# Performance work log

Hardware: AMD Instinct MI355X
Metric: run time of the kernel (lower is better)

## Reference

```python
import jax, jax.numpy as jnp
import numpy as np

N_NODES = 50000
EPS = 1e-5


def sage_conv_max(x, src, dst, W_l, b_l, W_r):
    # PyG SAGEConv(aggr='max'): out = lin_l(max_j x_j) + lin_r(x_i)
    msg = x[src]                                   # [E, d] gather
    agg = jnp.full((x.shape[0], x.shape[1]), -jnp.inf, dtype=x.dtype)
    agg = agg.at[dst].max(msg)                     # scatter-max over edges
    agg = jnp.where(jnp.isneginf(agg), 0.0, agg)   # isolated nodes -> 0 (PyG convention)
    return agg @ W_l.T + b_l + x @ W_r.T


def batch_norm(x, gamma, beta):
    mean = jnp.mean(x, axis=0)
    var = jnp.var(x, axis=0)
    return (x - mean) * jax.lax.rsqrt(var + EPS) * gamma + beta


def setup_inputs() -> dict:
    key = jax.random.key(0)
    ks = jax.random.split(key, 10)
    d_in, d_h, d_out = 128, 128, 32
    s = lambda fan: 1.0 / np.sqrt(fan)
    return {
        "x": jax.random.normal(ks[0], (N_NODES, d_in), dtype=jnp.float32),
        "edge_index": jax.random.randint(ks[1], (2, 800000), 0, N_NODES, dtype=jnp.int32),
        "W_l1": jax.random.uniform(ks[2], (d_h, d_in), jnp.float32, -s(d_in), s(d_in)),
        "b_l1": jnp.zeros((d_h,), jnp.float32),
        "W_r1": jax.random.uniform(ks[3], (d_h, d_in), jnp.float32, -s(d_in), s(d_in)),
        "gamma1": jnp.ones((d_h,), jnp.float32),
        "beta1": jnp.zeros((d_h,), jnp.float32),
        "W_l2": jax.random.uniform(ks[4], (d_out, d_h), jnp.float32, -s(d_h), s(d_h)),
        "b_l2": jnp.zeros((d_out,), jnp.float32),
        "W_r2": jax.random.uniform(ks[5], (d_out, d_h), jnp.float32, -s(d_h), s(d_h)),
    }


def reference(x, edge_index, W_l1, b_l1, W_r1, gamma1, beta1, W_l2, b_l2, W_r2):
    src, dst = edge_index[0], edge_index[1]
    h = sage_conv_max(x, src, dst, W_l1, b_l1, W_r1)
    h = batch_norm(h, gamma1, beta1)
    h = jax.nn.relu(h)
    # dropout is identity at inference
    return sage_conv_max(h, src, dst, W_l2, b_l2, W_r2)
```

## Files before the change

### kernel.cpp

```cpp
#include <hip/hip_runtime.h>
#include <math.h>
#include <float.h>

#define N_NODES 50000
#define N_EDGES 800000
#define DH 128
#define NB 196
#define EB 4096
#define NBUCK 98
#define BSH 9
#define CAP 80
#define SEGC 9216
#define CELLS_PER_BUCKET (NB * CAP)

typedef __attribute__((ext_vector_type(8))) short bf16x8;
typedef __attribute__((ext_vector_type(4))) float f32x4;

static __device__ __forceinline__ unsigned short f2bf(float f) {
  unsigned int u = __float_as_uint(f);
  u = (u + 0x7fff + ((u >> 16) & 1)) >> 16;
  return (unsigned short)u;
}

__global__ __launch_bounds__(256) void setup_kernel(
    const int* __restrict__ src, const int* __restrict__ dst,
    unsigned int* __restrict__ pairs,
    const float* __restrict__ x, const float* __restrict__ Wl1,
    const float* __restrict__ Wr1, const float* __restrict__ Wl2,
    const float* __restrict__ Wr2, unsigned int* __restrict__ x_bf,
    unsigned short* __restrict__ Wcat1, unsigned short* __restrict__ Wcat2,
    float* __restrict__ gsums) {
  const int b = blockIdx.x, tid = threadIdx.x;
  if (b < NB) {
    __shared__ int cur[NBUCK];
    if (tid < NBUCK) cur[tid] = 0;
    __syncthreads();
#pragma unroll
    for (int it = 0; it < EB / 256; ++it) {
      int e = b * EB + it * 256 + tid;
      if (e < N_EDGES) {
        int d = dst[e];
        int bk = d >> BSH;
        int p = atomicAdd(&cur[bk], 1);
        if (p < CAP)
          pairs[(size_t)(bk * NB + b) * CAP + p] =
              (unsigned)src[e] | ((unsigned)(d & 511) << 16);
      }
    }
    __syncthreads();
    for (int s = tid; s < NBUCK * CAP; s += 256) {
      int bk = s / CAP, slot = s - bk * CAP;
      if (slot >= cur[bk])
        pairs[(size_t)(bk * NB + b) * CAP + slot] = 0x80000000u;
    }
  } else if (b < NB + 6250) {
    int i = (b - NB) * 256 + tid;
    float4 v = ((const float4*)x)[i];
    uint2 o;
    o.x = (unsigned int)f2bf(v.x) | ((unsigned int)f2bf(v.y) << 16);
    o.y = (unsigned int)f2bf(v.z) | ((unsigned int)f2bf(v.w) << 16);
    ((uint2*)x_bf)[i] = o;
  } else if (b < NB + 6410) {
    int i = (b - NB - 6250) * 256 + tid;
    if (i < 32768) {
      int n = i >> 8, k = i & 255;
      float w = (k < 128) ? Wl1[n * 128 + k] : Wr1[n * 128 + (k - 128)];
      Wcat1[i] = f2bf(w);
    } else if (i < 40960) {
      int j = i - 32768;
      int n = j >> 8, k = j & 255;
      float w = (k < 128) ? Wl2[n * 128 + k] : Wr2[n * 128 + (k - 128)];
      Wcat2[j] = f2bf(w);
    }
  } else {
#pragma unroll
    for (int i = 0; i < 8; ++i) gsums[i * 256 + tid] = 0.f;
  }
}

__global__ __launch_bounds__(1024) void bucket_sort(const unsigned int* __restrict__ pairs,
                                                    unsigned int* __restrict__ rowinfo,
                                                    int* __restrict__ elist) {
  __shared__ int hist[512], sc[512], cpos[512];
  const int b = blockIdx.x, tid = threadIdx.x;
  const size_t s0 = (size_t)b * CELLS_PER_BUCKET;
  if (tid < 512) hist[tid] = 0;
  __syncthreads();
  for (int p = tid; p < CELLS_PER_BUCKET; p += 1024) {
    unsigned int pr = pairs[s0 + p];
    if ((int)pr >= 0) atomicAdd(&hist[(pr >> 16) & 511], 1);
  }
  __syncthreads();
  if (tid < 512) sc[tid] = hist[tid];
  __syncthreads();
  for (int off = 1; off < 512; off <<= 1) {
    int x = (tid < 512 && tid >= off) ? sc[tid - off] : 0;
    __syncthreads();
    if (tid < 512) sc[tid] += x;
    __syncthreads();
  }
  if (tid < 512) {
    int excl = sc[tid] - hist[tid];
    cpos[tid] = excl;
    int node = (b << BSH) + tid;
    if (node < N_NODES)
      rowinfo[node] = (unsigned)(b * SEGC + excl) | ((unsigned)hist[tid] << 20);
  }
  __syncthreads();
  for (int p = tid; p < CELLS_PER_BUCKET; p += 1024) {
    unsigned int pr = pairs[s0 + p];
    if ((int)pr >= 0) {
      int loc = atomicAdd(&cpos[(pr >> 16) & 511], 1);
      elist[b * SEGC + loc] = (int)(pr & 0xffffu);
    }
  }
}

template <bool BN>
__global__ __launch_bounds__(256) void agg_max_bf16(const uint4* __restrict__ feat4,
                                                    const unsigned int* __restrict__ rowinfo,
                                                    const int* __restrict__ elist,
                                                    const float* __restrict__ gsums,
                                                    const float* __restrict__ gamma,
                                                    const float* __restrict__ beta,
                                                    uint4* __restrict__ out4) {
  __shared__ float s_scale[128], s_shift[128];
  if (BN) {
    int t = threadIdx.x;
    if (t < 128) {
      float sm = 0.f, sq = 0.f;
#pragma unroll
      for (int r = 0; r < 8; ++r) {
        sm += gsums[r * 256 + t];
        sq += gsums[r * 256 + 128 + t];
      }
      const float inv = 1.f / (float)N_NODES;
      float mean = sm * inv;
      float var = sq * inv - mean * mean;
      float sc = gamma[t] * rsqrtf(var + 1e-5f);
      s_scale[t] = sc;
      s_shift[t] = beta[t] - mean * sc;
    }
    __syncthreads();
  }

  int node = blockIdx.x * 4 + (threadIdx.x >> 6);
  int lane = threadIdx.x & 63;
  int eslot = lane >> 4;
  int fq = lane & 15;
  unsigned int info = rowinfo[node];
  int e0 = (int)(info & 0xFFFFFu);
  int deg = (int)(info >> 20);
  int e1 = e0 + deg;
  float m[8];
#pragma unroll
  for (int j = 0; j < 8; ++j) m[j] = -FLT_MAX;

  if (deg > 0) {
    const int last = e1 - 1;
    for (int base = e0; base < e1; base += 16) {
      int idx[4];
#pragma unroll
      for (int q = 0; q < 4; ++q) {
        int e = base + q * 4 + eslot;
        if (e > last) e = last;
        idx[q] = elist[e];
      }
      uint4 v[4];
#pragma unroll
      for (int q = 0; q < 4; ++q) v[q] = feat4[(size_t)idx[q] * 16 + fq];
#pragma unroll
      for (int q = 0; q < 4; ++q) {
        const unsigned int* pv = (const unsigned int*)&v[q];
#pragma unroll
        for (int c = 0; c < 4; ++c) {
          m[2 * c]     = fmaxf(m[2 * c],     __uint_as_float(pv[c] << 16));
          m[2 * c + 1] = fmaxf(m[2 * c + 1], __uint_as_float(pv[c] & 0xffff0000u));
        }
      }
    }
  }

#pragma unroll
  for (int j = 0; j < 8; ++j) {
    m[j] = fmaxf(m[j], __shfl_xor(m[j], 16, 64));
    m[j] = fmaxf(m[j], __shfl_xor(m[j], 32, 64));
  }
  if (eslot == 0) {
    if (deg == 0) {
#pragma unroll
      for (int j = 0; j < 8; ++j) m[j] = 0.f;
    } else if (BN) {
#pragma unroll
      for (int j = 0; j < 8; ++j) {
        int col = fq * 8 + j;
        m[j] = fmaxf(m[j] * s_scale[col] + s_shift[col], 0.f);
      }
    }
    uint4 o;
    o.x = (unsigned)f2bf(m[0]) | ((unsigned)f2bf(m[1]) << 16);
    o.y = (unsigned)f2bf(m[2]) | ((unsigned)f2bf(m[3]) << 16);
    o.z = (unsigned)f2bf(m[4]) | ((unsigned)f2bf(m[5]) << 16);
    o.w = (unsigned)f2bf(m[6]) | ((unsigned)f2bf(m[7]) << 16);
    out4[(size_t)node * 16 + fq] = o;
  }
}

#define ASTR 264

template <int NT, bool BF16OUT, bool STATS, bool BNIN>
__global__ __launch_bounds__(256) void gemm_mfma(
    const unsigned short* __restrict__ Aa, const unsigned short* __restrict__ Ab,
    const unsigned short* __restrict__ Wcat, const float* __restrict__ bias,
    unsigned short* __restrict__ outb, float* __restrict__ outf,
    float* __restrict__ gsums, const float* __restrict__ gamma,
    const float* __restrict__ beta, int N) {
  __shared__ unsigned short Alds[128 * ASTR];
  __shared__ float s_sum[128], s_sq[128];
  __shared__ float s_scale[128], s_shift[128];
  const int tid = threadIdx.x;
  const int rowBase = blockIdx.x * 128;

  if (STATS && tid < 128) { s_sum[tid] = 0.f; s_sq[tid] = 0.f; }
  if (BNIN) {
    if (tid < 128) {
      float sm = 0.f, sq = 0.f;
#pragma unroll
      for (int r = 0; r < 8; ++r) {
        sm += gsums[r * 256 + tid];
        sq += gsums[r * 256 + 128 + tid];
      }
      const float inv = 1.f / (float)N_NODES;
      float mean = sm * inv;
      float var = sq * inv - mean * mean;
      float sc = gamma[tid] * rsqrtf(var + 1e-5f);
      s_scale[tid] = sc;
      s_shift[tid] = beta[tid] - mean * sc;
    }
    __syncthreads();
  }

#pragma unroll
  for (int it = 0; it < 16; ++it) {
    int f = tid + it * 256;
    int r = f >> 5;
    int seg = f & 31;
    int n = rowBase + r;
    if (n >= N) n = N - 1;
    const unsigned short* src = (seg < 16)
        ? (Aa + (size_t)n * 128 + seg * 8)
        : (Ab + (size_t)n * 128 + (seg - 16) * 8);
    int4 d = *(const int4*)src;
    if (BNIN && seg >= 16) {
      int kb = (seg - 16) * 8;
      unsigned int* dp = (unsigned int*)&d;
#pragma unroll
      for (int c = 0; c < 4; ++c) {
        int k0 = kb + 2 * c;
        float lo = __uint_as_float(dp[c] << 16);
        float hi = __uint_as_float(dp[c] & 0xffff0000u);
        lo = fmaxf(lo * s_scale[k0] + s_shift[k0], 0.f);
        hi = fmaxf(hi * s_scale[k0 + 1] + s_shift[k0 + 1], 0.f);
        dp[c] = (unsigned)f2bf(lo) | ((unsigned)f2bf(hi) << 16);
      }
    }
    *(int4*)(&Alds[r * ASTR + seg * 8]) = d;
  }
  __syncthreads();

  const int wv = tid >> 6;
  const int lane = tid & 63;
  const int ln15 = lane & 15;
  const int quad = lane >> 4;
  const int m0 = wv * 32;

  f32x4 acc[2][NT] = {};

#pragma unroll
  for (int ks = 0; ks < 8; ++ks) {
    const int k0 = ks * 32;
    bf16x8 a0 = *(const bf16x8*)(&Alds[(m0 + ln15) * ASTR + k0 + quad * 8]);
    bf16x8 a1 = *(const bf16x8*)(&Alds[(m0 + 16 + ln15) * ASTR + k0 + quad * 8]);
#pragma unroll
    for (int nt = 0; nt < NT; ++nt) {
      bf16x8 b = *(const bf16x8*)(Wcat + (size_t)(nt * 16 + ln15) * 256 + k0 + quad * 8);
      acc[0][nt] = __builtin_amdgcn_mfma_f32_16x16x32_bf16(a0, b, acc[0][nt], 0, 0, 0);
      acc[1][nt] = __builtin_amdgcn_mfma_f32_16x16x32_bf16(a1, b, acc[1][nt], 0, 0, 0);
    }
  }

  const int ldo = NT * 16;
#pragma unroll
  for (int nt = 0; nt < NT; ++nt) {
    int col = nt * 16 + ln15;
    float bv = bias[col];
    float psum = 0.f, psq = 0.f;
#pragma unroll
    for (int mt = 0; mt < 2; ++mt) {
#pragma unroll
      for (int i = 0; i < 4; ++i) {
        int r = rowBase + m0 + mt * 16 + quad * 4 + i;
        if (r < N) {
          float val = acc[mt][nt][i] + bv;
          if (STATS) { psum += val; psq += val * val; }
          if (BF16OUT)
            outb[(size_t)r * ldo + col] = f2bf(val);
          else
            outf[(size_t)r * ldo + col] = val;
        }
      }
    }
    if (STATS) {
      atomicAdd(&s_sum[col], psum);
      atomicAdd(&s_sq[col], psq);
    }
  }
  if (STATS) {
    __syncthreads();
    if (tid < 128) {
      int rep = blockIdx.x & 7;
      atomicAdd(&gsums[rep * 256 + tid], s_sum[tid]);
      atomicAdd(&gsums[rep * 256 + 128 + tid], s_sq[tid]);
    }
  }
}

extern "C" void kernel_launch(void* const* d_in, const int* in_sizes, int n_in,
                              void* d_out, int out_size, void* d_ws, size_t ws_size,
                              hipStream_t stream) {
  (void)in_sizes; (void)n_in; (void)out_size; (void)ws_size;
  const float* x     = (const float*)d_in[0];
  const int*   eidx  = (const int*)d_in[1];
  const float* W_l1  = (const float*)d_in[2];
  const float* b_l1  = (const float*)d_in[3];
  const float* W_r1  = (const float*)d_in[4];
  const float* gamma = (const float*)d_in[5];
  const float* beta  = (const float*)d_in[6];
  const float* W_l2  = (const float*)d_in[7];
  const float* b_l2  = (const float*)d_in[8];
  const float* W_r2  = (const float*)d_in[9];
  const int* srcp = eidx;
  const int* dstp = eidx + N_EDGES;
  float* out = (float*)d_out;

  int* wsi = (int*)d_ws;
  float* gsums   = (float*)wsi;
  unsigned int* rowinfo = (unsigned int*)(wsi + 2048);
  int*   elist   = wsi + 52064;
  unsigned int* pairs   = (unsigned int*)(wsi + 955232);
  unsigned int* x_bf    = (unsigned int*)(wsi + 2491872);
  unsigned int* agg_bf  = (unsigned int*)(wsi + 5691872);
  unsigned int* h_bf    = (unsigned int*)(wsi + 8891872);
  unsigned short* Wcat1 = (unsigned short*)(wsi + 12091872);
  unsigned short* Wcat2 = (unsigned short*)(wsi + 12108256);

  setup_kernel<<<dim3(NB + 6410 + 1), 256, 0, stream>>>(
      srcp, dstp, pairs, x, W_l1, W_r1, W_l2, W_r2, x_bf, Wcat1, Wcat2, gsums);

  bucket_sort<<<dim3(NBUCK), 1024, 0, stream>>>(pairs, rowinfo, elist);

  agg_max_bf16<false><<<dim3(N_NODES / 4), 256, 0, stream>>>(
      (const uint4*)x_bf, rowinfo, elist, nullptr, nullptr, nullptr, (uint4*)agg_bf);
  gemm_mfma<8, true, true, false><<<dim3(391), 256, 0, stream>>>(
      (const unsigned short*)agg_bf, (const unsigned short*)x_bf, Wcat1, b_l1,
      (unsigned short*)h_bf, nullptr, gsums, nullptr, nullptr, N_NODES);

  agg_max_bf16<true><<<dim3(N_NODES / 4), 256, 0, stream>>>(
      (const uint4*)h_bf, rowinfo, elist, gsums, gamma, beta, (uint4*)agg_bf);
  gemm_mfma<2, false, false, true><<<dim3(391), 256, 0, stream>>>(
      (const unsigned short*)agg_bf, (const unsigned short*)h_bf, Wcat2, b_l2,
      nullptr, out, gsums, gamma, beta, N_NODES);
}
```

Before: 222.4 us.

## Use finer dst buckets, per-cell counts instead of sentinel padding, and wave-shuffle scan

Doubles the number of destination buckets (256 nodes each, 196 blocks) and halves edges per setup block, so bucket_sort runs on more blocks with smaller histograms. The setup kernel now writes a per-cell count instead of filling unused slots with a sentinel, and bucket_sort reads only valid slots using those counts. The 512-element shared-memory Hillis-Steele scan is replaced by a wave-level shuffle scan with a small cross-wave fixup. The risk is tighter per-cell capacity (36 slots), which could drop edges if a cell overflows.

```diff
diff --git a/kernel.cpp b/kernel.cpp
--- a/kernel.cpp
+++ b/kernel.cpp
@@ -4,13 +4,12 @@
 
 #define N_NODES 50000
 #define N_EDGES 800000
-#define DH 128
-#define NB 196
-#define EB 4096
-#define NBUCK 98
-#define BSH 9
-#define CAP 80
-#define SEGC 9216
+#define NB 392
+#define EB 2048
+#define NBUCK 196
+#define BSH 8
+#define CAP 36
+#define SEGC 4864
 #define CELLS_PER_BUCKET (NB * CAP)
 
 typedef __attribute__((ext_vector_type(8))) short bf16x8;
@@ -24,7 +23,7 @@
 
 __global__ __launch_bounds__(256) void setup_kernel(
     const int* __restrict__ src, const int* __restrict__ dst,
-    unsigned int* __restrict__ pairs,
+    unsigned int* __restrict__ pairs, int* __restrict__ counts,
     const float* __restrict__ x, const float* __restrict__ Wl1,
     const float* __restrict__ Wr1, const float* __restrict__ Wl2,
     const float* __restrict__ Wr2, unsigned int* __restrict__ x_bf,
@@ -44,14 +43,13 @@
         int p = atomicAdd(&cur[bk], 1);
         if (p < CAP)
           pairs[(size_t)(bk * NB + b) * CAP + p] =
-              (unsigned)src[e] | ((unsigned)(d & 511) << 16);
-      }
-    }
-    __syncthreads();
-    for (int s = tid; s < NBUCK * CAP; s += 256) {
-      int bk = s / CAP, slot = s - bk * CAP;
-      if (slot >= cur[bk])
-        pairs[(size_t)(bk * NB + b) * CAP + slot] = 0x80000000u;
+              (unsigned)src[e] | ((unsigned)(d & 255) << 16);
+      }
+    }
+    __syncthreads();
+    if (tid < NBUCK) {
+      int c = cur[tid];
+      counts[tid * NB + b] = c > CAP ? CAP : c;
     }
   } else if (b < NB + 6250) {
     int i = (b - NB) * 256 + tid;
@@ -79,38 +77,62 @@
 }
 
 __global__ __launch_bounds__(1024) void bucket_sort(const unsigned int* __restrict__ pairs,
+                                                    const int* __restrict__ counts,
                                                     unsigned int* __restrict__ rowinfo,
                                                     int* __restrict__ elist) {
-  __shared__ int hist[512], sc[512], cpos[512];
+  __shared__ int hist[256], cpos[256], cnt[NB];
+  __shared__ int wsum[4];
   const int b = blockIdx.x, tid = threadIdx.x;
   const size_t s0 = (size_t)b * CELLS_PER_BUCKET;
-  if (tid < 512) hist[tid] = 0;
+  if (tid < 256) hist[tid] = 0;
+  if (tid < NB) cnt[tid] = counts[b * NB + tid];
   __syncthreads();
   for (int p = tid; p < CELLS_PER_BUCKET; p += 1024) {
-    unsigned int pr = pairs[s0 + p];
-    if ((int)pr >= 0) atomicAdd(&hist[(pr >> 16) & 511], 1);
-  }
-  __syncthreads();
-  if (tid < 512) sc[tid] = hist[tid];
-  __syncthreads();
-  for (int off = 1; off < 512; off <<= 1) {
-    int x = (tid < 512 && tid >= off) ? sc[tid - off] : 0;
-    __syncthreads();
-    if (tid < 512) sc[tid] += x;
-    __syncthreads();
-  }
-  if (tid < 512) {
-    int excl = sc[tid] - hist[tid];
+    int c = p / CAP, s = p - c * CAP;
+    if (s < cnt[c]) {
+      unsigned int pr = pairs[s0 + p];
+      atomicAdd(&hist[(pr >> 16) & 255], 1);
+    }
+  }
+  __syncthreads();
+  int incl = 0, h = 0;
+  if (tid < 256) {
+    const int l = tid & 63;
+    h = hist[tid];
+    incl = h;
+#pragma unroll
+    for (int off = 1; off < 64; off <<= 1) {
+      int t = __shfl_up(incl, off, 64);
+      if (l >= off) incl += t;
+    }
+    if (l == 63) wsum[tid >> 6] = incl;
+  }
+  __syncthreads();
+  if (tid < 64) {
+    int v = (tid < 4) ? wsum[tid] : 0;
+#pragma unroll
+    for (int off = 1; off < 4; off <<= 1) {
+      int t = __shfl_up(v, off, 64);
+      if (tid >= off) v += t;
+    }
+    if (tid < 4) wsum[tid] = v;
+  }
+  __syncthreads();
+  if (tid < 256) {
+    const int w = tid >> 6;
+    int tot = incl + ((w > 0) ? wsum[w - 1] : 0);
+    int excl = tot - h;
     cpos[tid] = excl;
     int node = (b << BSH) + tid;
     if (node < N_NODES)
-      rowinfo[node] = (unsigned)(b * SEGC + excl) | ((unsigned)hist[tid] << 20);
+      rowinfo[node] = (unsigned)(b * SEGC + excl) | ((unsigned)h << 20);
   }
   __syncthreads();
   for (int p = tid; p < CELLS_PER_BUCKET; p += 1024) {
-    unsigned int pr = pairs[s0 + p];
-    if ((int)pr >= 0) {
-      int loc = atomicAdd(&cpos[(pr >> 16) & 511], 1);
+    int c = p / CAP, s = p - c * CAP;
+    if (s < cnt[c]) {
+      unsigned int pr = pairs[s0 + p];
+      int loc = atomicAdd(&cpos[(pr >> 16) & 255], 1);
       elist[b * SEGC + loc] = (int)(pr & 0xffffu);
     }
   }
@@ -346,18 +368,19 @@
   int* wsi = (int*)d_ws;
   float* gsums   = (float*)wsi;
   unsigned int* rowinfo = (unsigned int*)(wsi + 2048);
-  int*   elist   = wsi + 52064;
-  unsigned int* pairs   = (unsigned int*)(wsi + 955232);
-  unsigned int* x_bf    = (unsigned int*)(wsi + 2491872);
-  unsigned int* agg_bf  = (unsigned int*)(wsi + 5691872);
-  unsigned int* h_bf    = (unsigned int*)(wsi + 8891872);
-  unsigned short* Wcat1 = (unsigned short*)(wsi + 12091872);
-  unsigned short* Wcat2 = (unsigned short*)(wsi + 12108256);
+  int*   counts  = wsi + 52224;
+  int*   elist   = wsi + 129056;
+  unsigned int* pairs   = (unsigned int*)(wsi + 1082400);
+  unsigned int* x_bf    = (unsigned int*)(wsi + 3848352);
+  unsigned int* agg_bf  = (unsigned int*)(wsi + 7048352);
+  unsigned int* h_bf    = (unsigned int*)(wsi + 10248352);
+  unsigned short* Wcat1 = (unsigned short*)(wsi + 13448352);
+  unsigned short* Wcat2 = (unsigned short*)(wsi + 13464736);
 
   setup_kernel<<<dim3(NB + 6410 + 1), 256, 0, stream>>>(
-      srcp, dstp, pairs, x, W_l1, W_r1, W_l2, W_r2, x_bf, Wcat1, Wcat2, gsums);
-
-  bucket_sort<<<dim3(NBUCK), 1024, 0, stream>>>(pairs, rowinfo, elist);
+      srcp, dstp, pairs, counts, x, W_l1, W_r1, W_l2, W_r2, x_bf, Wcat1, Wcat2, gsums);
+
+  bucket_sort<<<dim3(NBUCK), 1024, 0, stream>>>(pairs, counts, rowinfo, elist);
 
   agg_max_bf16<false><<<dim3(N_NODES / 4), 256, 0, stream>>>(
       (const uint4*)x_bf, rowinfo, elist, nullptr, nullptr, nullptr, (uint4*)agg_bf);
```

Result: faster. 215.7 us (-3.0%).
